# Kernel tuning notes

Hardware: AMD Instinct MI355X
Metric: run time of the kernel (lower is better)

## Reference

```python
import math
import jax, jax.numpy as jnp
import numpy as np

B, S, D, H, DFF, MEM = 4, 1024, 1024, 16, 4096, 256
HD = D // H  # 64
EPS = 1e-5


def _ln(x, g, b):
    mu = jnp.mean(x, axis=-1, keepdims=True)
    var = jnp.mean(jnp.square(x - mu), axis=-1, keepdims=True)
    return (x - mu) * jax.lax.rsqrt(var + EPS) * g + b


def _rope(x, cos, sin):
    # x: (b, h, s, hd); cos/sin: (>=s, hd//2)
    s = x.shape[2]
    xp = x.reshape(*x.shape[:-1], -1, 2)
    x0, x1 = xp[..., 0], xp[..., 1]
    c = cos[:s][None, None]
    sn = sin[:s][None, None]
    r0 = x0 * c - x1 * sn
    r1 = x0 * sn + x1 * c
    return jnp.stack([r0, r1], axis=-1).reshape(x.shape)


def setup_inputs() -> dict:
    key = jax.random.key(0)
    ks = jax.random.split(key, 16)
    p = lambda k, shape: jax.random.normal(k, shape, dtype=jnp.float32) * 0.02

    tgt = jax.random.normal(ks[0], (B, S, D), dtype=jnp.float32)
    memory = jax.random.normal(ks[1], (B, MEM, D), dtype=jnp.float32)

    # causal additive mask (s, s)
    tgt_mask = jnp.where(jnp.tril(jnp.ones((S, S), bool)), 0.0, -1e9).astype(jnp.float32)

    # RoPE freqs, theta=10000
    inv_freq = 1.0 / (10000.0 ** (np.arange(0, HD, 2, dtype=np.float32) / HD))
    ang = np.arange(S, dtype=np.float32)[:, None] * inv_freq[None, :]
    rope_cos = jnp.asarray(np.cos(ang))
    rope_sin = jnp.asarray(np.sin(ang))

    return {
        "tgt": tgt, "memory": memory, "tgt_mask": tgt_mask,
        "rope_cos": rope_cos, "rope_sin": rope_sin,
        "qkv_w": p(ks[2], (3 * D, D)), "qkv_b": jnp.zeros((3 * D,), jnp.float32),
        "out_w": p(ks[3], (D, D)), "out_b": jnp.zeros((D,), jnp.float32),
        "ca_in_w": p(ks[4], (3 * D, D)), "ca_in_b": jnp.zeros((3 * D,), jnp.float32),
        "ca_out_w": p(ks[5], (D, D)), "ca_out_b": jnp.zeros((D,), jnp.float32),
        "ffn_w1": p(ks[6], (DFF, D)), "ffn_b1": jnp.zeros((DFF,), jnp.float32),
        "ffn_w2": p(ks[7], (D, DFF)), "ffn_b2": jnp.zeros((D,), jnp.float32),
        "ln1_g": jnp.ones((D,), jnp.float32), "ln1_b": jnp.zeros((D,), jnp.float32),
        "ln2_g": jnp.ones((D,), jnp.float32), "ln2_b": jnp.zeros((D,), jnp.float32),
        "ln3_g": jnp.ones((D,), jnp.float32), "ln3_b": jnp.zeros((D,), jnp.float32),
    }


def reference(tgt, memory, tgt_mask, rope_cos, rope_sin,
              qkv_w, qkv_b, out_w, out_b,
              ca_in_w, ca_in_b, ca_out_w, ca_out_b,
              ffn_w1, ffn_b1, ffn_w2, ffn_b2,
              ln1_g, ln1_b, ln2_g, ln2_b, ln3_g, ln3_b):
    b, s, d = tgt.shape
    scale = 1.0 / math.sqrt(HD)

    # ---- self-attention with RoPE ----
    x = _ln(tgt, ln1_g, ln1_b)
    qkv = (x @ qkv_w.T + qkv_b).reshape(b, s, 3, H, HD)
    qkv = jnp.transpose(qkv, (2, 0, 3, 1, 4))  # (3, b, h, s, hd)
    q, k, v = qkv[0], qkv[1], qkv[2]
    q = _rope(q, rope_cos, rope_sin)
    k = _rope(k, rope_cos, rope_sin)
    attn = jnp.einsum('bhqd,bhkd->bhqk', q, k) * scale
    attn = attn + tgt_mask[None, None]
    attn = jax.nn.softmax(attn, axis=-1)
    sa = jnp.einsum('bhqk,bhkd->bhqd', attn, v)
    sa = jnp.transpose(sa, (0, 2, 1, 3)).reshape(b, s, d)
    tgt = tgt + (sa @ out_w.T + out_b)

    # ---- cross-attention (standard MHA, no positional encoding) ----
    x = _ln(tgt, ln2_g, ln2_b)
    wq, wk, wv = jnp.split(ca_in_w, 3, axis=0)
    bq, bk, bv = jnp.split(ca_in_b, 3, axis=0)
    m = memory.shape[1]
    cq = (x @ wq.T + bq).reshape(b, s, H, HD).transpose(0, 2, 1, 3)
    ck = (memory @ wk.T + bk).reshape(b, m, H, HD).transpose(0, 2, 1, 3)
    cv = (memory @ wv.T + bv).reshape(b, m, H, HD).transpose(0, 2, 1, 3)
    cattn = jax.nn.softmax(jnp.einsum('bhqd,bhkd->bhqk', cq, ck) * scale, axis=-1)
    co = jnp.einsum('bhqk,bhkd->bhqd', cattn, cv)
    co = jnp.transpose(co, (0, 2, 1, 3)).reshape(b, s, d)
    tgt = tgt + (co @ ca_out_w.T + ca_out_b)

    # ---- FFN (exact GELU, as torch nn.GELU default) ----
    x = _ln(tgt, ln3_g, ln3_b)
    ff = jax.nn.gelu(x @ ffn_w1.T + ffn_b1, approximate=False) @ ffn_w2.T + ffn_b2
    return tgt + ff
```

## Files before the change

### kernel.cpp

```cpp
#include <hip/hip_runtime.h>
#include <hip/hip_bf16.h>


using bf16 = __hip_bfloat16;
typedef __bf16 bf16x8 __attribute__((ext_vector_type(8)));
typedef float f32x4 __attribute__((ext_vector_type(4)));

static constexpr int Bn = 4, Ssz = 1024, Dm = 1024, Hh = 16, HDd = 64, DFFn = 4096, MEMn = 256;

__device__ inline float bf2f(bf16 x) { return __bfloat162float(x); }
__device__ inline bf16 f2bf(float x) { return __float2bfloat16(x); }

__global__ void detect_kernel(const unsigned* __restrict__ cosw, int* __restrict__ flag) {
  if (threadIdx.x == 0) *flag = (cosw[0] == 0x3F800000u) ? 1 : 0;
}

struct CanonArgs {
  const void* src[23];
  void* dst[23];
  int n[23];
};
__global__ __launch_bounds__(256) void canon_all(CanonArgs a, float* __restrict__ resid,
                                                 const int* __restrict__ flagp) {
  const int seg = blockIdx.y;
  const int n4 = a.n[seg] >> 2;
  if (n4 == 0) return;
  const int fl = *flagp;
  if (fl) {
    const float4* s = (const float4*)a.src[seg];
    bf16* d = (bf16*)a.dst[seg];
    for (int i = blockIdx.x * 256 + threadIdx.x; i < n4; i += gridDim.x * 256) {
      float4 v = s[i];
      bf16 t[4] = {f2bf(v.x), f2bf(v.y), f2bf(v.z), f2bf(v.w)};
      *reinterpret_cast<unsigned long long*>(d + i * 4) =
          *reinterpret_cast<unsigned long long*>(t);
      if (seg == 0) *reinterpret_cast<float4*>(resid + i * 4) = v;
    }
  } else {
    const unsigned long long* s = (const unsigned long long*)a.src[seg];
    unsigned long long* d = (unsigned long long*)a.dst[seg];
    for (int i = blockIdx.x * 256 + threadIdx.x; i < n4; i += gridDim.x * 256) {
      unsigned long long v = s[i];
      d[i] = v;
      if (seg == 0) {
        const unsigned short* u = reinterpret_cast<const unsigned short*>(&v);
        float4 f;
        f.x = __uint_as_float(((unsigned)u[0]) << 16);
        f.y = __uint_as_float(((unsigned)u[1]) << 16);
        f.z = __uint_as_float(((unsigned)u[2]) << 16);
        f.w = __uint_as_float(((unsigned)u[3]) << 16);
        *reinterpret_cast<float4*>(resid + i * 4) = f;
      }
    }
  }
}

__global__ __launch_bounds__(256) void ln_kernel(const float* __restrict__ x,
                                                 const bf16* __restrict__ g,
                                                 const bf16* __restrict__ bb,
                                                 bf16* __restrict__ y) {
  const int row = blockIdx.x;
  const float* xr = x + (size_t)row * Dm;
  const int i0 = threadIdx.x * 4;
  float4 v = *reinterpret_cast<const float4*>(xr + i0);
  float s = v.x + v.y + v.z + v.w;
  float ss = v.x * v.x + v.y * v.y + v.z * v.z + v.w * v.w;
#pragma unroll
  for (int o = 32; o > 0; o >>= 1) {
    s += __shfl_down(s, o);
    ss += __shfl_down(ss, o);
  }
  __shared__ float shs[4], shss[4];
  const int wave = threadIdx.x >> 6, lane = threadIdx.x & 63;
  if (lane == 0) { shs[wave] = s; shss[wave] = ss; }
  __syncthreads();
  s = shs[0] + shs[1] + shs[2] + shs[3];
  ss = shss[0] + shss[1] + shss[2] + shss[3];
  const float mu = s * (1.0f / Dm);
  const float var = fmaxf(ss * (1.0f / Dm) - mu * mu, 0.0f);
  const float rs = rsqrtf(var + 1e-5f);
  bf16* yr = y + (size_t)row * Dm + i0;
  float vv[4] = {v.x, v.y, v.z, v.w};
#pragma unroll
  for (int j = 0; j < 4; ++j)
    yr[j] = f2bf((vv[j] - mu) * rs * bf2f(g[i0 + j]) + bf2f(bb[i0 + j]));
}

__global__ __launch_bounds__(256) void gemm_bt(
    const bf16* __restrict__ A, const bf16* __restrict__ W,
    const bf16* __restrict__ bias, bf16* __restrict__ outB, float* __restrict__ outF,
    const float* __restrict__ residIn, float* __restrict__ residOut,
    const int* __restrict__ flagp, int M, int N, int K, int epi) {
  __shared__ bf16 As[64][40];
  __shared__ bf16 Ws[64][40];
  const int tid = threadIdx.x;
  const int m0 = blockIdx.x * 64, n0 = blockIdx.y * 64;
  const int wave = tid >> 6, lane = tid & 63;
  const int wm = wave >> 1, wn = wave & 1;
  const int quad = lane >> 4, m16 = lane & 15;
  const int lr = tid >> 2, lc = (tid & 3) * 8;

  f32x4 acc[2][2] = {};

  const bf16* Ap = A + (size_t)(m0 + lr) * K + lc;
  const bf16* Wp = W + (size_t)(n0 + lr) * K + lc;
  for (int k0 = 0; k0 < K; k0 += 32) {
    float4 av = *reinterpret_cast<const float4*>(Ap + k0);
    float4 wv = *reinterpret_cast<const float4*>(Wp + k0);
    *reinterpret_cast<float4*>(&As[lr][lc]) = av;
    *reinterpret_cast<float4*>(&Ws[lr][lc]) = wv;
    __syncthreads();
    bf16x8 aF[2], bF[2];
#pragma unroll
    for (int t = 0; t < 2; ++t) {
      aF[t] = *reinterpret_cast<const bf16x8*>(&As[wm * 32 + t * 16 + m16][quad * 8]);
      bF[t] = *reinterpret_cast<const bf16x8*>(&Ws[wn * 32 + t * 16 + m16][quad * 8]);
    }
#pragma unroll
    for (int mt = 0; mt < 2; ++mt)
#pragma unroll
      for (int nt = 0; nt < 2; ++nt)
        acc[mt][nt] = __builtin_amdgcn_mfma_f32_16x16x32_bf16(aF[mt], bF[nt], acc[mt][nt], 0, 0, 0);
    __syncthreads();
  }
  const int fl = (epi == 3) ? *flagp : 0;
#pragma unroll
  for (int mt = 0; mt < 2; ++mt) {
#pragma unroll
    for (int nt = 0; nt < 2; ++nt) {
      const int col = n0 + wn * 32 + nt * 16 + m16;
      const float bv = bf2f(bias[col]);
#pragma unroll
      for (int r = 0; r < 4; ++r) {
        const int row = m0 + wm * 32 + mt * 16 + quad * 4 + r;
        const size_t idx = (size_t)row * N + col;
        float v = acc[mt][nt][r] + bv;
        if (epi == 0) {
          outB[idx] = f2bf(v);
        } else if (epi == 1) {
          outB[idx] = f2bf(0.5f * v * (1.0f + erff(v * 0.70710678118654752f)));
        } else if (epi == 2) {
          residOut[idx] = residIn[idx] + v;
        } else {
          const float rr = residIn[idx] + v;
          if (fl) outF[idx] = rr; else outB[idx] = f2bf(rr);
        }
      }
    }
  }
}

__global__ __launch_bounds__(256) void gemm128(
    const bf16* __restrict__ A, const bf16* __restrict__ W,
    const bf16* __restrict__ bias, bf16* __restrict__ outB, float* __restrict__ outF,
    const float* __restrict__ residIn, float* __restrict__ residOut,
    const int* __restrict__ flagp, int M, int N, int K, int epi) {
  __shared__ bf16 As[2][128][40];
  __shared__ bf16 Ws[2][128][40];
  const int tid = threadIdx.x;
  const int wave = tid >> 6, lane = tid & 63;
  const int wm = wave >> 1, wn = wave & 1;
  const int quad = lane >> 4, m16 = lane & 15;
  const int m0 = blockIdx.x * 128, n0 = blockIdx.y * 128;

  const int lr = tid >> 2;
  const int lc = (tid & 3) * 8;
  const bf16* Ap = A + (size_t)(m0 + lr) * K + lc;
  const bf16* Wp = W + (size_t)(n0 + lr) * K + lc;
  const size_t rowOff = (size_t)64 * K;

  f32x4 acc[4][4] = {};

  float4 ax0 = *reinterpret_cast<const float4*>(Ap);
  float4 ax1 = *reinterpret_cast<const float4*>(Ap + rowOff);
  float4 wx0 = *reinterpret_cast<const float4*>(Wp);
  float4 wx1 = *reinterpret_cast<const float4*>(Wp + rowOff);
  float4 ay0 = *reinterpret_cast<const float4*>(Ap + 32);
  float4 ay1 = *reinterpret_cast<const float4*>(Ap + rowOff + 32);
  float4 wy0 = *reinterpret_cast<const float4*>(Wp + 32);
  float4 wy1 = *reinterpret_cast<const float4*>(Wp + rowOff + 32);

  const int nsteps = K >> 5;
  for (int s = 0; s < nsteps; s += 2) {
    *reinterpret_cast<float4*>(&As[0][lr][lc]) = ax0;
    *reinterpret_cast<float4*>(&As[0][64 + lr][lc]) = ax1;
    *reinterpret_cast<float4*>(&Ws[0][lr][lc]) = wx0;
    *reinterpret_cast<float4*>(&Ws[0][64 + lr][lc]) = wx1;
    __syncthreads();
    if (s + 2 < nsteps) {
      const int k2 = (s + 2) * 32;
      ax0 = *reinterpret_cast<const float4*>(Ap + k2);
      ax1 = *reinterpret_cast<const float4*>(Ap + rowOff + k2);
      wx0 = *reinterpret_cast<const float4*>(Wp + k2);
      wx1 = *reinterpret_cast<const float4*>(Wp + rowOff + k2);
    }
    {
      bf16x8 aF[4], bF[4];
#pragma unroll
      for (int t = 0; t < 4; ++t) {
        aF[t] = *reinterpret_cast<const bf16x8*>(&As[0][wm * 64 + t * 16 + m16][quad * 8]);
        bF[t] = *reinterpret_cast<const bf16x8*>(&Ws[0][wn * 64 + t * 16 + m16][quad * 8]);
      }
#pragma unroll
      for (int mt = 0; mt < 4; ++mt)
#pragma unroll
        for (int nt = 0; nt < 4; ++nt)
          acc[mt][nt] = __builtin_amdgcn_mfma_f32_16x16x32_bf16(aF[mt], bF[nt], acc[mt][nt], 0, 0, 0);
    }
    *reinterpret_cast<float4*>(&As[1][lr][lc]) = ay0;
    *reinterpret_cast<float4*>(&As[1][64 + lr][lc]) = ay1;
    *reinterpret_cast<float4*>(&Ws[1][lr][lc]) = wy0;
    *reinterpret_cast<float4*>(&Ws[1][64 + lr][lc]) = wy1;
    __syncthreads();
    if (s + 3 < nsteps) {
      const int k3 = (s + 3) * 32;
      ay0 = *reinterpret_cast<const float4*>(Ap + k3);
      ay1 = *reinterpret_cast<const float4*>(Ap + rowOff + k3);
      wy0 = *reinterpret_cast<const float4*>(Wp + k3);
      wy1 = *reinterpret_cast<const float4*>(Wp + rowOff + k3);
    }
    {
      bf16x8 aF[4], bF[4];
#pragma unroll
      for (int t = 0; t < 4; ++t) {
        aF[t] = *reinterpret_cast<const bf16x8*>(&As[1][wm * 64 + t * 16 + m16][quad * 8]);
        bF[t] = *reinterpret_cast<const bf16x8*>(&Ws[1][wn * 64 + t * 16 + m16][quad * 8]);
      }
#pragma unroll
      for (int mt = 0; mt < 4; ++mt)
#pragma unroll
        for (int nt = 0; nt < 4; ++nt)
          acc[mt][nt] = __builtin_amdgcn_mfma_f32_16x16x32_bf16(aF[mt], bF[nt], acc[mt][nt], 0, 0, 0);
    }
  }
  const int fl = (epi == 3) ? *flagp : 0;
#pragma unroll
  for (int mt = 0; mt < 4; ++mt) {
#pragma unroll
    for (int nt = 0; nt < 4; ++nt) {
      const int col = n0 + wn * 64 + nt * 16 + m16;
      const float bv = bf2f(bias[col]);
#pragma unroll
      for (int r = 0; r < 4; ++r) {
        const int row = m0 + wm * 64 + mt * 16 + quad * 4 + r;
        const size_t idx = (size_t)row * N + col;
        float v = acc[mt][nt][r] + bv;
        if (epi == 0) {
          outB[idx] = f2bf(v);
        } else if (epi == 1) {
          outB[idx] = f2bf(0.5f * v * (1.0f + erff(v * 0.70710678118654752f)));
        } else if (epi == 2) {
          residOut[idx] = residIn[idx] + v;
        } else {
          const float rr = residIn[idx] + v;
          if (fl) outF[idx] = rr; else outB[idx] = f2bf(rr);
        }
      }
    }
  }
}

__global__ __launch_bounds__(256) void rope_kernel(bf16* __restrict__ qkv,
                                                   const bf16* __restrict__ cosb,
                                                   const bf16* __restrict__ sinb) {
  const int idx = blockIdx.x * 256 + threadIdx.x;
  const int i = idx & 31;
  const int h = (idx >> 5) & 15;
  const int r = idx >> 9;
  const int s = r & (Ssz - 1);
  const float c = bf2f(cosb[s * 32 + i]);
  const float sn = bf2f(sinb[s * 32 + i]);
  bf16* base = qkv + (size_t)r * (3 * Dm) + h * 64 + 2 * i;
  float x0 = bf2f(base[0]), x1 = bf2f(base[1]);
  base[0] = f2bf(x0 * c - x1 * sn);
  base[1] = f2bf(x0 * sn + x1 * c);
  x0 = bf2f(base[Dm]); x1 = bf2f(base[Dm + 1]);
  base[Dm] = f2bf(x0 * c - x1 * sn);
  base[Dm + 1] = f2bf(x0 * sn + x1 * c);
}

__global__ __launch_bounds__(256) void attn_mfma(
    const bf16* __restrict__ Qb, const bf16* __restrict__ Kb, const bf16* __restrict__ Vb,
    bf16* __restrict__ Ob, int qStride, int kvStride, int kvLen, int causal, float scale) {
  __shared__ bf16 Ks[64][72];
  __shared__ bf16 Vt[64][72];
  __shared__ bf16 Ps[64][72];
  const int tid = threadIdx.x;
  const int wave = tid >> 6, lane = tid & 63;
  const int quad = lane >> 4, m16 = lane & 15;
  const int b = blockIdx.z, h = blockIdx.y;
  const int q0 = blockIdx.x * 64;
  const int sr = tid >> 2, sc = (tid & 3) * 16;

  {
    const bf16* qp = Qb + (size_t)(b * Ssz + q0 + sr) * qStride + h * 64 + sc;
    float4 a = reinterpret_cast<const float4*>(qp)[0];
    float4 bb2 = reinterpret_cast<const float4*>(qp)[1];
    *reinterpret_cast<float4*>(&Ps[sr][sc]) = a;
    *reinterpret_cast<float4*>(&Ps[sr][sc + 8]) = bb2;
  }
  __syncthreads();
  bf16x8 qf[2];
  qf[0] = *reinterpret_cast<const bf16x8*>(&Ps[wave * 16 + m16][quad * 8]);
  qf[1] = *reinterpret_cast<const bf16x8*>(&Ps[wave * 16 + m16][32 + quad * 8]);

  f32x4 oacc[4] = {};
  float mrow[4], lrow[4];
#pragma unroll
  for (int r = 0; r < 4; ++r) { mrow[r] = -30000.0f; lrow[r] = 0.0f; }

  const int nk = causal ? (q0 + 64) : kvLen;
  for (int kt = 0; kt < nk; kt += 64) {
    {
      const bf16* kp = Kb + (size_t)(b * kvLen + kt + sr) * kvStride + h * 64 + sc;
      float4 k1 = reinterpret_cast<const float4*>(kp)[0];
      float4 k2 = reinterpret_cast<const float4*>(kp)[1];
      *reinterpret_cast<float4*>(&Ks[sr][sc]) = k1;
      *reinterpret_cast<float4*>(&Ks[sr][sc + 8]) = k2;
      const bf16* vp = Vb + (size_t)(b * kvLen + kt + sr) * kvStride + h * 64 + sc;
      float4 v1 = reinterpret_cast<const float4*>(vp)[0];
      float4 v2 = reinterpret_cast<const float4*>(vp)[1];
      const bf16* tv1 = reinterpret_cast<const bf16*>(&v1);
      const bf16* tv2 = reinterpret_cast<const bf16*>(&v2);
#pragma unroll
      for (int j = 0; j < 8; ++j) {
        Vt[sc + j][sr] = tv1[j];
        Vt[sc + 8 + j][sr] = tv2[j];
      }
    }
    __syncthreads();

    f32x4 sacc[4] = {};
#pragma unroll
    for (int nt = 0; nt < 4; ++nt) {
      bf16x8 kf0 = *reinterpret_cast<const bf16x8*>(&Ks[nt * 16 + m16][quad * 8]);
      bf16x8 kf1 = *reinterpret_cast<const bf16x8*>(&Ks[nt * 16 + m16][32 + quad * 8]);
      sacc[nt] = __builtin_amdgcn_mfma_f32_16x16x32_bf16(qf[0], kf0, sacc[nt], 0, 0, 0);
      sacc[nt] = __builtin_amdgcn_mfma_f32_16x16x32_bf16(qf[1], kf1, sacc[nt], 0, 0, 0);
    }
    const bool dmask = (causal != 0) && (kt == q0);
#pragma unroll
    for (int nt = 0; nt < 4; ++nt) {
#pragma unroll
      for (int r = 0; r < 4; ++r) {
        float s = sacc[nt][r] * scale;
        if (dmask && (nt * 16 + m16 > wave * 16 + quad * 4 + r)) s = -30000.0f;
        sacc[nt][r] = s;
      }
    }

#pragma unroll
    for (int r = 0; r < 4; ++r) {
      float mx = fmaxf(fmaxf(sacc[0][r], sacc[1][r]), fmaxf(sacc[2][r], sacc[3][r]));
#pragma unroll
      for (int off = 1; off < 16; off <<= 1) mx = fmaxf(mx, __shfl_xor(mx, off));
      const float mn = fmaxf(mrow[r], mx);
      const float corr = __expf(mrow[r] - mn);
      mrow[r] = mn;
      float psum = 0.0f;
#pragma unroll
      for (int nt = 0; nt < 4; ++nt) {
        const float p = __expf(sacc[nt][r] - mn);
        sacc[nt][r] = p;
        psum += p;
      }
#pragma unroll
      for (int off = 1; off < 16; off <<= 1) psum += __shfl_xor(psum, off);
      lrow[r] = lrow[r] * corr + psum;
#pragma unroll
      for (int nt = 0; nt < 4; ++nt) oacc[nt][r] *= corr;
#pragma unroll
      for (int nt = 0; nt < 4; ++nt)
        Ps[wave * 16 + quad * 4 + r][nt * 16 + m16] = f2bf(sacc[nt][r]);
    }
    bf16x8 pf0 = *reinterpret_cast<const bf16x8*>(&Ps[wave * 16 + m16][quad * 8]);
    bf16x8 pf1 = *reinterpret_cast<const bf16x8*>(&Ps[wave * 16 + m16][32 + quad * 8]);
#pragma unroll
    for (int nt = 0; nt < 4; ++nt) {
      bf16x8 vf0 = *reinterpret_cast<const bf16x8*>(&Vt[nt * 16 + m16][quad * 8]);
      bf16x8 vf1 = *reinterpret_cast<const bf16x8*>(&Vt[nt * 16 + m16][32 + quad * 8]);
      oacc[nt] = __builtin_amdgcn_mfma_f32_16x16x32_bf16(pf0, vf0, oacc[nt], 0, 0, 0);
      oacc[nt] = __builtin_amdgcn_mfma_f32_16x16x32_bf16(pf1, vf1, oacc[nt], 0, 0, 0);
    }
    __syncthreads();
  }

  float inv[4];
#pragma unroll
  for (int r = 0; r < 4; ++r) inv[r] = 1.0f / lrow[r];
#pragma unroll
  for (int r = 0; r < 4; ++r) {
    bf16* op = Ob + (size_t)(b * Ssz + q0 + wave * 16 + quad * 4 + r) * Dm + h * 64 + m16;
#pragma unroll
    for (int nt = 0; nt < 4; ++nt) op[nt * 16] = f2bf(oacc[nt][r] * inv[r]);
  }
}

extern "C" void kernel_launch(void* const* d_in, const int* in_sizes, int n_in,
                              void* d_out, int out_size, void* d_ws, size_t ws_size,
                              hipStream_t stream) {
  char* ws = (char*)d_ws;
  int* flagp   = (int*)ws;
  float* resid = (float*)(ws + (1ull << 20));
  bf16* xln    = (bf16*)(ws + (17ull << 20));
  bf16* aout   = (bf16*)(ws + (25ull << 20));
  bf16* big    = (bf16*)(ws + (33ull << 20));
  size_t off   = (65ull << 20);

  detect_kernel<<<1, 64, 0, stream>>>((const unsigned*)d_in[3], flagp);

  CanonArgs ca;
  bf16* c[23];
  for (int i = 0; i < 23; ++i) {
    if (i == 2) { c[i] = nullptr; ca.src[i] = d_in[i]; ca.dst[i] = nullptr; ca.n[i] = 0; continue; }
    c[i] = (bf16*)(ws + off);
    const int n = in_sizes[i];
    off += ((size_t)n * 2 + 255) & ~(size_t)255;
    ca.src[i] = d_in[i];
    ca.dst[i] = c[i];
    ca.n[i] = n;
  }
  canon_all<<<dim3(256, 23), 256, 0, stream>>>(ca, resid, flagp);

  const bf16 *memory = c[1], *rope_cos = c[3], *rope_sin = c[4];
  const bf16 *qkv_w = c[5], *qkv_b = c[6], *out_w = c[7], *out_b = c[8];
  const bf16 *ca_in_w = c[9], *ca_in_b = c[10], *ca_out_w = c[11], *ca_out_b = c[12];
  const bf16 *ffn_w1 = c[13], *ffn_b1 = c[14], *ffn_w2 = c[15], *ffn_b2 = c[16];
  const bf16 *ln1_g = c[17], *ln1_b = c[18], *ln2_g = c[19], *ln2_b = c[20];
  const bf16 *ln3_g = c[21], *ln3_b = c[22];

  bf16* qb = big;
  bf16* kb = (bf16*)(ws + (41ull << 20));
  bf16* vb = (bf16*)(ws + (43ull << 20));
  bf16* outB = (bf16*)d_out;
  float* outF = (float*)d_out;

  const int ROWS = Bn * Ssz;
  const float scale = 0.125f;

  ln_kernel<<<ROWS, 256, 0, stream>>>(resid, ln1_g, ln1_b, xln);
  gemm128<<<dim3(ROWS / 128, (3 * Dm) / 128), 256, 0, stream>>>(
      xln, qkv_w, qkv_b, big, nullptr, nullptr, nullptr, nullptr, ROWS, 3 * Dm, Dm, 0);
  rope_kernel<<<(ROWS * Hh * (HDd / 2)) / 256, 256, 0, stream>>>(big, rope_cos, rope_sin);
  attn_mfma<<<dim3(Ssz / 64, Hh, Bn), 256, 0, stream>>>(
      big, big + Dm, big + 2 * Dm, aout, 3 * Dm, 3 * Dm, Ssz, 1, scale);
  gemm128<<<dim3(ROWS / 128, Dm / 128), 256, 0, stream>>>(
      aout, out_w, out_b, nullptr, nullptr, resid, resid, nullptr, ROWS, Dm, Dm, 2);

  ln_kernel<<<ROWS, 256, 0, stream>>>(resid, ln2_g, ln2_b, xln);
  gemm128<<<dim3(ROWS / 128, Dm / 128), 256, 0, stream>>>(
      xln, ca_in_w, ca_in_b, qb, nullptr, nullptr, nullptr, nullptr, ROWS, Dm, Dm, 0);
  gemm_bt<<<dim3((Bn * MEMn) / 64, Dm / 64), 256, 0, stream>>>(
      memory, ca_in_w + (size_t)Dm * Dm, ca_in_b + Dm, kb, nullptr, nullptr, nullptr, nullptr,
      Bn * MEMn, Dm, Dm, 0);
  gemm_bt<<<dim3((Bn * MEMn) / 64, Dm / 64), 256, 0, stream>>>(
      memory, ca_in_w + (size_t)2 * Dm * Dm, ca_in_b + 2 * Dm, vb, nullptr, nullptr, nullptr, nullptr,
      Bn * MEMn, Dm, Dm, 0);
  attn_mfma<<<dim3(Ssz / 64, Hh, Bn), 256, 0, stream>>>(
      qb, kb, vb, aout, Dm, Dm, MEMn, 0, scale);
  gemm128<<<dim3(ROWS / 128, Dm / 128), 256, 0, stream>>>(
      aout, ca_out_w, ca_out_b, nullptr, nullptr, resid, resid, nullptr, ROWS, Dm, Dm, 2);

  ln_kernel<<<ROWS, 256, 0, stream>>>(resid, ln3_g, ln3_b, xln);
  gemm128<<<dim3(ROWS / 128, DFFn / 128), 256, 0, stream>>>(
      xln, ffn_w1, ffn_b1, big, nullptr, nullptr, nullptr, nullptr, ROWS, DFFn, Dm, 1);
  gemm128<<<dim3(ROWS / 128, Dm / 128), 256, 0, stream>>>(
      big, ffn_w2, ffn_b2, outB, outF, resid, nullptr, flagp, ROWS, Dm, DFFn, 3);
}
```

Before: 573.0 us.

## Load GEMM tiles directly into LDS via global_load_lds, single buffer

Replaces the register-staged, double-buffered tile loading in the 128x128 GEMM with direct global-to-LDS loads, using 16-byte global_load_lds transfers into a single unpadded LDS buffer. The aim is to drop the VGPR staging and the LDS store instructions. In exchange, the kernel loses prefetch overlap between loading the next K-slice and running MFMAs, and adds a second barrier per step. Removing the row padding may also cause LDS bank conflicts on the fragment reads.

Result: slower. 657.0 us (+14.6%).

```diff
diff --git a/kernel.cpp b/kernel.cpp
--- a/kernel.cpp
+++ b/kernel.cpp
@@ -10,6 +10,12 @@
 
 __device__ inline float bf2f(bf16 x) { return __bfloat162float(x); }
 __device__ inline bf16 f2bf(float x) { return __float2bfloat16(x); }
+
+__device__ __forceinline__ void gload16(const bf16* g, bf16* l) {
+  __builtin_amdgcn_global_load_lds(
+      (const __attribute__((address_space(1))) void*)g,
+      (__attribute__((address_space(3))) void*)l, 16, 0, 0);
+}
 
 __global__ void detect_kernel(const unsigned* __restrict__ cosw, int* __restrict__ flag) {
   if (threadIdx.x == 0) *flag = (cosw[0] == 0x3F800000u) ? 1 : 0;
@@ -155,84 +161,42 @@
     const bf16* __restrict__ bias, bf16* __restrict__ outB, float* __restrict__ outF,
     const float* __restrict__ residIn, float* __restrict__ residOut,
     const int* __restrict__ flagp, int M, int N, int K, int epi) {
-  __shared__ bf16 As[2][128][40];
-  __shared__ bf16 Ws[2][128][40];
+  __shared__ bf16 As[128][32];
+  __shared__ bf16 Ws[128][32];
   const int tid = threadIdx.x;
   const int wave = tid >> 6, lane = tid & 63;
   const int wm = wave >> 1, wn = wave & 1;
   const int quad = lane >> 4, m16 = lane & 15;
   const int m0 = blockIdx.x * 128, n0 = blockIdx.y * 128;
 
-  const int lr = tid >> 2;
-  const int lc = (tid & 3) * 8;
-  const bf16* Ap = A + (size_t)(m0 + lr) * K + lc;
-  const bf16* Wp = W + (size_t)(n0 + lr) * K + lc;
+  const int sr = tid >> 2;
+  const int sc = (tid & 3) * 8;
+  const bf16* Ap = A + (size_t)(m0 + sr) * K + sc;
+  const bf16* Wp = W + (size_t)(n0 + sr) * K + sc;
   const size_t rowOff = (size_t)64 * K;
 
   f32x4 acc[4][4] = {};
 
-  float4 ax0 = *reinterpret_cast<const float4*>(Ap);
-  float4 ax1 = *reinterpret_cast<const float4*>(Ap + rowOff);
-  float4 wx0 = *reinterpret_cast<const float4*>(Wp);
-  float4 wx1 = *reinterpret_cast<const float4*>(Wp + rowOff);
-  float4 ay0 = *reinterpret_cast<const float4*>(Ap + 32);
-  float4 ay1 = *reinterpret_cast<const float4*>(Ap + rowOff + 32);
-  float4 wy0 = *reinterpret_cast<const float4*>(Wp + 32);
-  float4 wy1 = *reinterpret_cast<const float4*>(Wp + rowOff + 32);
-
-  const int nsteps = K >> 5;
-  for (int s = 0; s < nsteps; s += 2) {
-    *reinterpret_cast<float4*>(&As[0][lr][lc]) = ax0;
-    *reinterpret_cast<float4*>(&As[0][64 + lr][lc]) = ax1;
-    *reinterpret_cast<float4*>(&Ws[0][lr][lc]) = wx0;
-    *reinterpret_cast<float4*>(&Ws[0][64 + lr][lc]) = wx1;
-    __syncthreads();
-    if (s + 2 < nsteps) {
-      const int k2 = (s + 2) * 32;
-      ax0 = *reinterpret_cast<const float4*>(Ap + k2);
-      ax1 = *reinterpret_cast<const float4*>(Ap + rowOff + k2);
-      wx0 = *reinterpret_cast<const float4*>(Wp + k2);
-      wx1 = *reinterpret_cast<const float4*>(Wp + rowOff + k2);
-    }
-    {
-      bf16x8 aF[4], bF[4];
-#pragma unroll
-      for (int t = 0; t < 4; ++t) {
-        aF[t] = *reinterpret_cast<const bf16x8*>(&As[0][wm * 64 + t * 16 + m16][quad * 8]);
-        bF[t] = *reinterpret_cast<const bf16x8*>(&Ws[0][wn * 64 + t * 16 + m16][quad * 8]);
-      }
-#pragma unroll
-      for (int mt = 0; mt < 4; ++mt)
-#pragma unroll
-        for (int nt = 0; nt < 4; ++nt)
-          acc[mt][nt] = __builtin_amdgcn_mfma_f32_16x16x32_bf16(aF[mt], bF[nt], acc[mt][nt], 0, 0, 0);
-    }
-    *reinterpret_cast<float4*>(&As[1][lr][lc]) = ay0;
-    *reinterpret_cast<float4*>(&As[1][64 + lr][lc]) = ay1;
-    *reinterpret_cast<float4*>(&Ws[1][lr][lc]) = wy0;
-    *reinterpret_cast<float4*>(&Ws[1][64 + lr][lc]) = wy1;
-    __syncthreads();
-    if (s + 3 < nsteps) {
-      const int k3 = (s + 3) * 32;
-      ay0 = *reinterpret_cast<const float4*>(Ap + k3);
-      ay1 = *reinterpret_cast<const float4*>(Ap + rowOff + k3);
-      wy0 = *reinterpret_cast<const float4*>(Wp + k3);
-      wy1 = *reinterpret_cast<const float4*>(Wp + rowOff + k3);
-    }
-    {
-      bf16x8 aF[4], bF[4];
-#pragma unroll
-      for (int t = 0; t < 4; ++t) {
-        aF[t] = *reinterpret_cast<const bf16x8*>(&As[1][wm * 64 + t * 16 + m16][quad * 8]);
-        bF[t] = *reinterpret_cast<const bf16x8*>(&Ws[1][wn * 64 + t * 16 + m16][quad * 8]);
-      }
-#pragma unroll
-      for (int mt = 0; mt < 4; ++mt)
-#pragma unroll
-        for (int nt = 0; nt < 4; ++nt)
-          acc[mt][nt] = __builtin_amdgcn_mfma_f32_16x16x32_bf16(aF[mt], bF[nt], acc[mt][nt], 0, 0, 0);
-    }
-  }
+  for (int k0 = 0; k0 < K; k0 += 32) {
+    gload16(Ap + k0, &As[sr][sc]);
+    gload16(Ap + rowOff + k0, &As[64 + sr][sc]);
+    gload16(Wp + k0, &Ws[sr][sc]);
+    gload16(Wp + rowOff + k0, &Ws[64 + sr][sc]);
+    __syncthreads();
+    bf16x8 aF[4], bF[4];
+#pragma unroll
+    for (int t = 0; t < 4; ++t) {
+      aF[t] = *reinterpret_cast<const bf16x8*>(&As[wm * 64 + t * 16 + m16][quad * 8]);
+      bF[t] = *reinterpret_cast<const bf16x8*>(&Ws[wn * 64 + t * 16 + m16][quad * 8]);
+    }
+#pragma unroll
+    for (int mt = 0; mt < 4; ++mt)
+#pragma unroll
+      for (int nt = 0; nt < 4; ++nt)
+        acc[mt][nt] = __builtin_amdgcn_mfma_f32_16x16x32_bf16(aF[mt], bF[nt], acc[mt][nt], 0, 0, 0);
+    __syncthreads();
+  }
+
   const int fl = (epi == 3) ? *flagp : 0;
 #pragma unroll
   for (int mt = 0; mt < 4; ++mt) {
```
